# Kernel tuning notes

Measured on AMD Instinct MI355X. Metric: run time of the kernel, lower is better.

Reference implementation:

```python
import jax, jax.numpy as jnp
import numpy as np

LMAX = 6; MMAX = 2
C = 128          # num_channels
H = 8            # num_heads
ALPHA = 32       # attn_alpha_channels
VAL = 16         # attn_value_channels (H*VAL == C)
HID = 64         # attn_hidden_channels
FFN = 128        # ffn_hidden_channels
NL = 4           # num_layers
CUTOFF = 12.0; NRBF = 600
AVG_DEG = 23.395238876342773
AVG_NODES = 77.81317
EPS = 1e-16

def _maps():
    idx, ls = [], []
    for l in range(LMAX + 1):
        mm = min(l, MMAX)
        for m in range(-mm, mm + 1):
            idx.append(l * l + l + m); ls.append(l)
    return np.array(idx), np.array(ls)
_M2F_np, _LOF_np = _maps()
M2F = jnp.asarray(_M2F_np)   # [KM] full-coefficient index of each m-restricted coeff
LOF = jnp.asarray(_LOF_np)   # [KM] degree l of each m-restricted coeff
KM = int(_M2F_np.shape[0])   # 29 for lmax=6, mmax=2
KF = (LMAX + 1) ** 2         # 49

def _rbf(d):
    # GaussianSmearing(0, cutoff, NRBF, width_scalar=2.0)
    off = jnp.linspace(0.0, CUTOFF, NRBF)
    coeff = -0.5 / (2.0 * (off[1] - off[0])) ** 2
    return jnp.exp(coeff * (d[:, None] - off) ** 2)

def _envelope(d):
    # PolynomialEnvelope, exponent p=5
    x = d / CUTOFF
    env = 1.0 - 21.0 * x ** 5 + 35.0 * x ** 6 - 15.0 * x ** 7
    return jnp.where(x < 1.0, env, 0.0)

def _rms(x, g):
    # merge-norm over channel dim with learned per-channel scale
    return x * jax.lax.rsqrt(jnp.mean(x * x, axis=-1, keepdims=True) + 1e-6) * g

def _forward(atomic_numbers, edge_index, edge_distance, emb,
             We0, be0, We1, be1, Weproj, gamma1, gamma2,
             Wr0, Wr1, Wrl, Wmsg, Wap, wa, Wg, Wv, Wo,
             Wf1, Wfg, Wf2, Wh1, Wh2):
    N = atomic_numbers.shape[0]
    src, tgt = edge_index[0], edge_index[1]
    rbf = _rbf(edge_distance)            # [E, NRBF]
    env = _envelope(edge_distance)       # [E]
    # node init: atom embedding on the l=0 component
    x = jnp.zeros((N, KF, C), rbf.dtype).at[:, 0, :].set(emb[atomic_numbers])
    # edge-degree embedding: radial MLP -> per-edge coeffs -> scatter to targets
    h = jax.nn.silu(rbf @ We0 + be0)
    h = jax.nn.silu(h @ We1 + be1)
    deg = (h @ Weproj).reshape(-1, KM, C)              # [E, KM, C]
    x = x.at[tgt[:, None], M2F[None, :], :].add(deg / AVG_DEG)
    for i in range(NL):
        # ---- equivariant graph attention ----
        y = _rms(x, gamma1[i])
        ym = y[:, M2F, :]                               # [N, KM, C] m-restricted
        m = jnp.concatenate([ym[src], ym[tgt]], axis=-1)  # [E, KM, 2C]
        m = jnp.einsum('ekc,ch->ekh', m, Wmsg[i])       # [E, KM, HID]
        # radial function, shared across m within each l (use_rad_l_parametrization)
        rad = jax.nn.silu(jax.nn.silu(rbf @ Wr0[i]) @ Wr1[i])
        radl = rad @ Wrl[i]                             # [E, LMAX+1]
        m = m * radl[:, LOF][..., None]
        # attention logits from invariant (l=0) part
        a = jax.nn.silu(m[:, 0, :] @ Wap[i]).reshape(-1, H, ALPHA)
        logits = jnp.einsum('eha,ha->eh', a, wa[i])     # [E, H]
        segmax = jnp.full((N, H), -jnp.inf, logits.dtype).at[tgt].max(logits)
        ex = env[:, None] * jnp.exp(logits - segmax[tgt])  # envelope-masked softmax
        den = jax.ops.segment_sum(ex, tgt, num_segments=N)
        attn = ex / (den[tgt] + EPS)                    # [E, H]
        # SwiGLU-gated equivariant values
        g = jax.nn.silu(m[:, 0, :] @ Wg[i])             # [E, H*VAL]
        v = jnp.einsum('ekh,hv->ekv', m, Wv[i]) * g[:, None, :]
        v = v.reshape(-1, KM, H, VAL) * attn[:, None, :, None]
        agg = jax.ops.segment_sum(v.reshape(-1, KM, H * VAL), tgt, num_segments=N)
        out = jnp.einsum('nkv,vc->nkc', agg, Wo[i])     # [N, KM, C]
        x = x.at[:, M2F, :].add(out)
        # ---- feed-forward (grid-MLP style SwiGLU) ----
        y = _rms(x, gamma2[i])
        gf = jax.nn.silu(y[:, 0, :] @ Wfg[i])           # [N, FFN]
        hf = jnp.einsum('nkc,cf->nkf', y, Wf1[i]) * gf[:, None, :]
        x = x + jnp.einsum('nkf,fc->nkc', hf, Wf2[i])
    # energy head on invariant part, sum-aggregated over nodes
    s = jax.nn.silu(x[:, 0, :] @ Wh1) @ Wh2             # [N, 1]
    return (jnp.sum(s) / AVG_NODES).reshape(1)

def setup_inputs() -> dict:
    key = jax.random.key(0)
    ks = jax.random.split(key, 24)
    N, E = 6000, 120000
    def rn(k, shape, scale=0.05):
        return jax.random.normal(k, shape, dtype=jnp.float32) * scale
    inp = {}
    inp['atomic_numbers'] = jax.random.randint(ks[0], (N,), 0, 128)
    inp['edge_index'] = jax.random.randint(ks[1], (2, E), 0, N)
    inp['edge_distance'] = jax.random.uniform(ks[2], (E,), minval=0.5, maxval=CUTOFF, dtype=jnp.float32)
    inp['emb'] = rn(ks[3], (128, C), 1.0)
    inp['We0'] = rn(ks[4], (NRBF, 128)); inp['be0'] = jnp.zeros((128,), jnp.float32)
    inp['We1'] = rn(ks[5], (128, 128)); inp['be1'] = jnp.zeros((128,), jnp.float32)
    inp['Weproj'] = rn(ks[6], (128, KM * C))
    inp['gamma1'] = jnp.ones((NL, C), jnp.float32)
    inp['gamma2'] = jnp.ones((NL, C), jnp.float32)
    inp['Wr0'] = rn(ks[7], (NL, NRBF, 128))
    inp['Wr1'] = rn(ks[8], (NL, 128, 128))
    inp['Wrl'] = rn(ks[9], (NL, 128, LMAX + 1), 0.1)
    inp['Wmsg'] = rn(ks[10], (NL, 2 * C, HID))
    inp['Wap'] = rn(ks[11], (NL, HID, H * ALPHA))
    inp['wa'] = rn(ks[12], (NL, H, ALPHA))
    inp['Wg'] = rn(ks[13], (NL, HID, H * VAL))
    inp['Wv'] = rn(ks[14], (NL, HID, H * VAL))
    inp['Wo'] = rn(ks[15], (NL, H * VAL, C))
    inp['Wf1'] = rn(ks[16], (NL, C, FFN))
    inp['Wfg'] = rn(ks[17], (NL, C, FFN))
    inp['Wf2'] = rn(ks[18], (NL, FFN, C))
    inp['Wh1'] = rn(ks[19], (C, C))
    inp['Wh2'] = rn(ks[20], (C, 1))
    return inp

def reference(atomic_numbers, edge_index, edge_distance, emb,
              We0, be0, We1, be1, Weproj, gamma1, gamma2,
              Wr0, Wr1, Wrl, Wmsg, Wap, wa, Wg, Wv, Wo,
              Wf1, Wfg, Wf2, Wh1, Wh2):
    return _forward(atomic_numbers, edge_index, edge_distance, emb,
                    We0, be0, We1, be1, Weproj, gamma1, gamma2,
                    Wr0, Wr1, Wrl, Wmsg, Wap, wa, Wg, Wv, Wo,
                    Wf1, Wfg, Wf2, Wh1, Wh2)
```

## Files before the change

### kernel.cpp

```cpp
#include <hip/hip_runtime.h>

#define KM 29
#define GTAB 2048

typedef __bf16 bf16_t;
typedef __bf16 bf16x8 __attribute__((ext_vector_type(8)));
typedef __bf16 bf16x4 __attribute__((ext_vector_type(4)));
typedef __bf16 bf16x2 __attribute__((ext_vector_type(2)));
typedef float  f32x4  __attribute__((ext_vector_type(4)));
typedef float  f32x2  __attribute__((ext_vector_type(2)));

__device__ __forceinline__ float silu_f(float x){ return x / (1.0f + __expf(-x)); }

__device__ __forceinline__ float wave_reduce_sum(float v){
  #pragma unroll
  for (int s = 1; s < 64; s <<= 1) v += __shfl_xor(v, s);
  return v;
}

__device__ __forceinline__ constexpr int LOF2(int k){
  return (k<1)?0 : (k<4)?1 : (k<9)?2 : (k<14)?3 : (k<19)?4 : (k<24)?5 : 6;
}

__device__ __forceinline__ f32x4 mfma16(bf16x8 a, bf16x8 b, f32x4 c){
// ... 91 lines not shown
  #pragma unroll
  for (int u = 0; u < 10; u++) p[u] = 0.f;
  const int c2 = 2*lane;
  for (int jj = 0; jj < 32; jj++){
    float gj = __shfl(gval, jj);
    int row = j0 + jj;
    const float2 w0 = *(const float2*)(We0 + row*128 + c2);
    p[0] += gj*w0.x; p[1] += gj*w0.y;
    #pragma unroll
    for (int i = 0; i < 4; i++){
      const float2 wr = *(const float2*)(Wr0 + ((size_t)i*600 + row)*128 + c2);
      p[2+2*i] += gj*wr.x; p[3+2*i] += gj*wr.y;
    }
  }
  sb[wid][c2]   = silu_f(p[0] + be0[c2]);
  sb[wid][c2+1] = silu_f(p[1] + be0[c2+1]);
  #pragma unroll
  for (int i = 0; i < 4; i++){
    sb[wid][128 + 128*i + c2]   = silu_f(p[2+2*i]);
    sb[wid][128 + 128*i + c2+1] = silu_f(p[3+2*i]);
  }
  float a0 = 0.f, a1 = 0.f;
  for (int c = 0; c < 128; c++){
    float hv = sb[wid][c];
    const float2 w = *(const float2*)(We1 + c*128 + c2);
    a0 += hv*w.x; a1 += hv*w.y;
  }
  a0 = silu_f(a0 + be1[c2]); a1 = silu_f(a1 + be1[c2+1]);
  h2tab[(size_t)e*128 + c2]     = a0;
  h2tab[(size_t)e*128 + c2 + 1] = a1;
  #pragma unroll
  for (int i = 0; i < 4; i++){
    float r0 = 0.f, r1 = 0.f;
    const float* W1 = Wr1 + (size_t)i*128*128;
    for (int c = 0; c < 128; c++){
      float rv = sb[wid][128 + 128*i + c];
      const float2 w = *(const float2*)(W1 + c*128 + c2);
      r0 += rv*w.x; r1 += rv*w.y;
    }
    r0 = silu_f(r0); r1 = silu_f(r1);
    const float* Wl = Wrl + (size_t)i*128*7;
    float pl[7];
    #pragma unroll
    for (int l = 0; l < 7; l++) pl[l] = r0*Wl[c2*7+l] + r1*Wl[(c2+1)*7+l];
    #pragma unroll
    for (int l = 0; l < 7; l++) pl[l] = wave_reduce_sum(pl[l]);
    if (lane == 0){
      #pragma unroll
      for (int l = 0; l < 7; l++) radtab[(size_t)e*28 + i*7 + l] = pl[l];
    }
  }
}

__global__ void k_h2e(const float* __restrict__ ed, const float* __restrict__ h2tab,
                      bf16_t* __restrict__ h2e, int E){
  int idx = blockIdx.x*256 + threadIdx.x;
  if (idx >= E*128) return;
  int e = idx >> 7, ch = idx & 127;
  float d = ed[e];
  float u = d * ((GTAB-1)/12.0f);
  int j = (int)u; if (j > GTAB-2) j = GTAB-2;
  float f = u - (float)j;
  float a = h2tab[(size_t)j*128 + ch], b = h2tab[(size_t)(j+1)*128 + ch];
  h2e[idx] = (bf16_t)(a + f*(b-a));
}

__global__ __launch_bounds__(256) void k_h2sum(
    const bf16_t* __restrict__ h2e, const int* __restrict__ rowptr, const int* __restrict__ order,
    bf16_t* __restrict__ h2sum, int N)
{
  int n = blockIdx.x*2 + (threadIdx.x >> 7);
  int ch = threadIdx.x & 127;
  if (n >= N) return;
  int rp = rowptr[n], deg = rowptr[n+1] - rp;
  float acc = 0.f;
  for (int idx = 0; idx < deg; idx++){
    int e = order[rp+idx];
    acc += (float)h2e[(size_t)e*128 + ch];
  }
  h2sum[(size_t)n*128 + ch] = (bf16_t)acc;
}

__global__ __launch_bounds__(256) void k_init_x(
    const int* __restrict__ Z, const float* __restrict__ emb,
    const bf16_t* __restrict__ WeprojT, const bf16_t* __restrict__ h2sum,
    bf16_t* __restrict__ Xb, int N)
{
  __shared__ bf16_t h2s[32*136];
  __shared__ int Zs[32];
  int n0 = blockIdx.x*32, t = threadIdx.x;
  for (int idx = t; idx < 32*128; idx += 256){
    int nn = idx >> 7, ch = idx & 127;
    int n = n0 + nn;
    h2s[nn*136 + ch] = (n < N) ? h2sum[(size_t)n*128 + ch] : (bf16_t)0.f;
  }
  if (t < 32) Zs[t] = (n0 + t < N) ? Z[n0+t] : 0;
  __syncthreads();
  int wid = t >> 6, lane = t & 63;
  int mtile = wid & 1;
  int row = mtile*16 + (lane & 15);
  int koff = (lane >> 4)*8;
  bf16x8 afr[4];
  #pragma unroll
  for (int kk = 0; kk < 4; kk++) afr[kk] = *(const bf16x8*)(h2s + row*136 + kk*32 + koff);
  for (int nt = (wid>>1); nt < 232; nt += 2){
    f32x4 acc = {0.f,0.f,0.f,0.f};
    int col = nt*16 + (lane & 15);
    #pragma unroll
    for (int kk = 0; kk < 4; kk++){
      bf16x8 b = *(const bf16x8*)(WeprojT + (size_t)col*128 + kk*32 + koff);
      acc = mfma16(afr[kk], b, acc);
    }
    #pragma unroll
    for (int r = 0; r < 4; r++){
      int r32 = mtile*16 + (lane>>4)*4 + r;
      int n = n0 + r32;
      if (n < N){
        float v = acc[r] * (1.0f/23.395238876342773f);
        if (col < 128) v += emb[(size_t)Zs[r32]*128 + col];
        Xb[(size_t)n*3712 + col] = (bf16_t)v;
      }
    }
  }
}

__global__ __launch_bounds__(512) void k_pqv(
    const bf16_t* __restrict__ Xb, const float* __restrict__ gamma1,
    const bf16_t* __restrict__ WmsgCT, const bf16_t* __restrict__ WvT,
    unsigned char* __restrict__ PV8, unsigned char* __restrict__ QV8,
    float* __restrict__ P0, float* __restrict__ Q0, int layer)
{
  __shared__ bf16_t ys16[32*136];
  __shared__ bf16_t pq16[32*136];
  int n = blockIdx.x, t = threadIdx.x;
  int wid = t >> 6, lane = t & 63;
  const float* g1 = gamma1 + layer*128;
  const bf16_t* xp = Xb + (size_t)n*3712;
  for (int k = wid; k < KM; k += 8){
    float x0 = (float)xp[k*128 + lane], x1 = (float)xp[k*128 + 64 + lane];
    float ss = wave_reduce_sum(x0*x0 + x1*x1);
    float sc = rsqrtf(ss*(1.0f/128.0f) + 1e-6f);
    ys16[k*136 + lane]      = (bf16_t)(x0*sc*g1[lane]);
    ys16[k*136 + 64 + lane] = (bf16_t)(x1*sc*g1[64+lane]);
  }
  for (int idx = t; idx < 3*136; idx += 512) ys16[29*136 + idx] = (bf16_t)0.f;
  __syncthreads();
  int mtile = wid >> 2;
  int row = mtile*16 + (lane & 15);
  int koff = (lane >> 4)*8;
  {
    const bf16_t* Bc = WmsgCT + (size_t)layer*16384;
    f32x4 acc[2] = {{0,0,0,0},{0,0,0,0}};
    #pragma unroll
    for (int kk = 0; kk < 128; kk += 32){
      bf16x8 a = *(const bf16x8*)(ys16 + row*136 + kk + koff);
      #pragma unroll
      for (int u = 0; u < 2; u++){
        int col = ((wid&3)*2+u)*16 + (lane & 15);
        bf16x8 b = *(const bf16x8*)(Bc + (size_t)col*128 + kk + koff);
        acc[u] = mfma16(a, b, acc[u]);
      }
    }
    #pragma unroll
    for (int u = 0; u < 2; u++){
      int col = ((wid&3)*2+u)*16 + (lane & 15);
      #pragma unroll
      for (int r = 0; r < 4; r++){
        int r32 = mtile*16 + (lane>>4)*4 + r;
        pq16[r32*136 + col] = (bf16_t)acc[u][r];
      }
      if (mtile == 0 && (lane>>4) == 0){
        float v = acc[u][0];
        if (col < 64) P0[(size_t)n*64 + col] = v;
        else          Q0[(size_t)n*64 + col - 64] = v;
      }
    }
  }
  __syncthreads();
  {
    const bf16_t* Bt = WvT + (size_t)layer*8192;
    f32x4 acc[2] = {{0,0,0,0},{0,0,0,0}};
    #pragma unroll
    for (int kk = 0; kk < 64; kk += 32){
      bf16x8 a = *(const bf16x8*)(pq16 + row*136 + kk + koff);
      #pragma unroll
      for (int u = 0; u < 2; u++){
        int col = ((wid&3)*2+u)*16 + (lane & 15);
        bf16x8 b = *(const bf16x8*)(Bt + (size_t)col*64 + kk + koff);
        acc[u] = mfma16(a, b, acc[u]);
      }
    }
    unsigned char* pvp = PV8 + (size_t)n*4096;
    int r0i = mtile*16 + (lane>>4)*4;
    #pragma unroll
    for (int u = 0; u < 2; u++){
      int col = ((wid&3)*2+u)*16 + (lane & 15);
      float pk[4];
      #pragma unroll
      for (int r = 0; r < 4; r++){
        int r32 = r0i + r;
        pk[r] = (r32 < KM) ? acc[u][r] : 0.f;
      }
      int dw = __builtin_amdgcn_cvt_pk_fp8_f32(pk[0], pk[1], 0, false);
      dw = __builtin_amdgcn_cvt_pk_fp8_f32(pk[2], pk[3], dw, true);
      *(unsigned int*)(pvp + col*32 + r0i) = (unsigned int)dw;
    }
  }
  {
    const bf16_t* Bt = WvT + (size_t)layer*8192;
    f32x4 acc[2] = {{0,0,0,0},{0,0,0,0}};
    #pragma unroll
    for (int kk = 0; kk < 64; kk += 32){
      bf16x8 a = *(const bf16x8*)(pq16 + row*136 + 64 + kk + koff);
      #pragma unroll
      for (int u = 0; u < 2; u++){
        int col = ((wid&3)*2+u)*16 + (lane & 15);
        bf16x8 b = *(const bf16x8*)(Bt + (size_t)col*64 + kk + koff);
        acc[u] = mfma16(a, b, acc[u]);
      }
    }
    unsigned char* qvp = QV8 + (size_t)n*4096;
    int r0i = mtile*16 + (lane>>4)*4;
    #pragma unroll
    for (int u = 0; u < 2; u++){
      int col = ((wid&3)*2+u)*16 + (lane & 15);
      float pk[4];
      #pragma unroll
      for (int r = 0; r < 4; r++){
        int r32 = r0i + r;
        pk[r] = (r32 < KM) ? acc[u][r] : 0.f;
      }
      int dw = __builtin_amdgcn_cvt_pk_fp8_f32(pk[0], pk[1], 0, false);
      dw = __builtin_amdgcn_cvt_pk_fp8_f32(pk[2], pk[3], dw, true);
      *(unsigned int*)(qvp + col*32 + r0i) = (unsigned int)dw;
    }
  }
}

__global__ __launch_bounds__(256) void k_edge_logits(
    const int* __restrict__ EI, const float* __restrict__ ed,
    const float* __restrict__ P0, const float* __restrict__ Q0,
    const float* __restrict__ radtab, const bf16_t* __restrict__ WapT, const float* __restrict__ wa,
    const bf16_t* __restrict__ WgT, float* __restrict__ logi, bf16_t* __restrict__ gate16,
    int E, int layer)
{
  __shared__ bf16_t m0s[16*72];
  __shared__ int   srcs[16], tgts[16];
  __shared__ float r0s[16];
  int t = threadIdx.x;
  int eb = blockIdx.x*16;
  if (t < 16){
    int e = eb + t;
    if (e < E){
      srcs[t] = EI[e]; tgts[t] = EI[E+e];
      float d = ed[e];
      float u = d * ((GTAB-1)/12.0f);
      int j = (int)u; if (j > GTAB-2) j = GTAB-2;
      float f = u - (float)j;
      float a = radtab[(size_t)j*28 + layer*7], b = radtab[(size_t)(j+1)*28 + layer*7];
      r0s[t] = a + f*(b-a);
    } else { srcs[t] = 0; tgts[t] = 0; r0s[t] = 0.f; }
  }
  __syncthreads();
  #pragma unroll
  for (int u = 0; u < 4; u++){
    int idx = t + u*256;
    int i = idx >> 6, j = idx & 63;
    m0s[i*72 + j] = (bf16_t)((P0[(size_t)srcs[i]*64 + j] + Q0[(size_t)tgts[i]*64 + j]) * r0s[i]);
  }
  __syncthreads();
  int wid = t >> 6, lane = t & 63;
  int l15 = lane & 15, lg = lane >> 4;
  int koff = lg*8;
  bf16x8 a0 = *(const bf16x8*)(m0s + l15*72 + koff);
  bf16x8 a1 = *(const bf16x8*)(m0s + l15*72 + 32 + koff);
  const bf16_t* Ba = WapT + (size_t)layer*16384;
  const bf16_t* Bg = WgT  + (size_t)layer*8192;
  const float* wav = wa + layer*256;
  f32x4 accA[4], accG[2];
  #pragma unroll
  for (int u = 0; u < 4; u++){
    int col = 64*wid + u*16 + l15;
    f32x4 acc = {0,0,0,0};
    acc = mfma16(a0, *(const bf16x8*)(Ba + (size_t)col*64 + koff), acc);
    acc = mfma16(a1, *(const bf16x8*)(Ba + (size_t)col*64 + 32 + koff), acc);
    accA[u] = acc;
  }
// ... 127 lines not shown
      A0 = B0; A1 = B1; gA = gB;
      B0 = C0; B1 = C1; gB = gC;
      i += 4;
    }
  }
  {
    const unsigned char* qvp = QV8 + (size_t)n*4096 + hv*32;
    uint4 q0 = *(const uint4*)qvp;
    uint4 q1 = *(const uint4*)(qvp + 16);
    float rw[7];
    #pragma unroll
    for (int l = 0; l < 7; l++) rw[l] = S[l];
    FMA_DW(q0.x, 0)  FMA_DW(q0.y, 4)  FMA_DW(q0.z, 8)  FMA_DW(q0.w, 12)
    FMA_DW(q1.x, 16) FMA_DW(q1.y, 20) FMA_DW(q1.z, 24) FMA_DW(q1.w, 28)
  }
  if ((hv & 15) == 0) denl[eg*8 + h] = dpart;
  __syncthreads();
  {
    float dsum = denl[h] + denl[8 + h] + denl[16 + h] + denl[24 + h];
    float inv = 1.0f/(dsum + 1e-30f);
    #pragma unroll
    for (int j = 0; j < 32; j++) acc[j] *= inv;
  }
  if (eg == 0){
    #pragma unroll
    for (int j = 0; j < 32; j++) mA[j*136 + hv] = (bf16_t)acc[j];
  } else if (eg == 1){
    #pragma unroll
    for (int j = 0; j < 32; j++) mB[j*136 + hv] = (bf16_t)acc[j];
  }
  __syncthreads();
  if (eg == 2){
    #pragma unroll
    for (int j = 0; j < 32; j++) mA[j*136 + hv] = (bf16_t)((float)mA[j*136 + hv] + acc[j]);
  } else if (eg == 3){
    #pragma unroll
    for (int j = 0; j < 32; j++) mB[j*136 + hv] = (bf16_t)((float)mB[j*136 + hv] + acc[j]);
  }
  __syncthreads();
  for (int idx = t; idx < 3712; idx += 512){
    int k = idx >> 7, c = idx & 127;
    agg[(size_t)n*3712 + idx] = (bf16_t)((float)mA[k*136 + c] + (float)mB[k*136 + c]);
  }
}

__global__ __launch_bounds__(512, 4) void k_xupdate(
    const bf16_t* __restrict__ agg,
    const float* __restrict__ gamma1, const float* __restrict__ gamma2,
    const float* __restrict__ Wfg,
    const bf16_t* __restrict__ Wf1T, const bf16_t* __restrict__ Wf2T,
    const bf16_t* __restrict__ WoT, const bf16_t* __restrict__ WmsgCT, const bf16_t* __restrict__ WvT,
    bf16_t* __restrict__ Xb, int layer,
    unsigned char* __restrict__ PV8o, unsigned char* __restrict__ QV8o,
    float* __restrict__ P0o, float* __restrict__ Q0o, int do_tail)
{
  __shared__ float  xs[3712];
  __shared__ bf16_t ysag[32*136];
  __shared__ bf16_t hsqv[32*136];
  __shared__ float  pf[640];

  int n = blockIdx.x, t = threadIdx.x;
  int wid = t >> 6, lane = t & 63;

  {
    const bf16x2* Xp2 = (const bf16x2*)(Xb + (size_t)n*3712);
    for (int p = t; p < 1856; p += 512){
      bf16x2 v = Xp2[p];
      xs[2*p]   = (float)v.x;
      xs[2*p+1] = (float)v.y;
    }
  }
  for (int idx = t; idx < 3712; idx += 512){
    int k = idx >> 7, c = idx & 127;
    ysag[k*136 + c] = agg[(size_t)n*3712 + idx];
  }
  for (int idx = t; idx < 3*136; idx += 512) ysag[29*136 + idx] = (bf16_t)0.f;
  __syncthreads();
  {
    const bf16_t* Bt = WoT + (size_t)layer*16384;
    int mtile = wid >> 2, colt = (wid & 3)*2;
    int row = mtile*16 + (lane & 15);
    int koff = (lane >> 4)*8;
    f32x4 a2[2] = {{0,0,0,0},{0,0,0,0}};
    #pragma unroll
    for (int kk = 0; kk < 128; kk += 32){
      bf16x8 a = *(const bf16x8*)(ysag + row*136 + kk + koff);
      #pragma unroll
      for (int u = 0; u < 2; u++){
        int col = (colt+u)*16 + (lane & 15);
        bf16x8 b = *(const bf16x8*)(Bt + (size_t)col*128 + kk + koff);
        a2[u] = mfma16(a, b, a2[u]);
      }
    }
    #pragma unroll
    for (int u = 0; u < 2; u++){
      int col = (colt+u)*16 + (lane & 15);
      #pragma unroll
      for (int r = 0; r < 4; r++){
        int r32 = mtile*16 + (lane>>4)*4 + r;
        if (r32 < KM) xs[r32*128 + col] += a2[u][r];
      }
    }
  }
  __syncthreads();
  const float* g2 = gamma2 + layer*128;
  for (int k = wid; k < KM; k += 8){
    float x0 = xs[k*128 + lane], x1 = xs[k*128 + 64 + lane];
    float ss = wave_reduce_sum(x0*x0 + x1*x1);
    float sc = rsqrtf(ss*(1.0f/128.0f) + 1e-6f);
    ysag[k*136 + lane]      = (bf16_t)(x0*sc*g2[lane]);
    ysag[k*136 + 64 + lane] = (bf16_t)(x1*sc*g2[64+lane]);
  }
  for (int idx = t; idx < 3*136; idx += 512) ysag[29*136 + idx] = (bf16_t)0.f;
  __syncthreads();
  {
    int part = t >> 7, f = t & 127;
    const float* Wfgp = Wfg + (size_t)layer*16384;
    float p = 0.f;
    for (int c = part*32; c < part*32 + 32; c++) p += (float)ysag[c] * Wfgp[c*128 + f];
    pf[part*128 + f] = p;
  }
  __syncthreads();
  if (t < 128) pf[512 + t] = silu_f(pf[t] + pf[128+t] + pf[256+t] + pf[384+t]);
  __syncthreads();
  {
    const bf16_t* Bt = Wf1T + (size_t)layer*16384;
    int mtile = wid >> 2, colt = (wid & 3)*2;
    int row = mtile*16 + (lane & 15);
    int koff = (lane >> 4)*8;
    f32x4 a2[2] = {{0,0,0,0},{0,0,0,0}};
    #pragma unroll
    for (int kk = 0; kk < 128; kk += 32){
      bf16x8 a = *(const bf16x8*)(ysag + row*136 + kk + koff);
      #pragma unroll
      for (int u = 0; u < 2; u++){
        int col = (colt+u)*16 + (lane & 15);
        bf16x8 b = *(const bf16x8*)(Bt + (size_t)col*128 + kk + koff);
        a2[u] = mfma16(a, b, a2[u]);
      }
    }
    #pragma unroll
    for (int u = 0; u < 2; u++){
      int col = (colt+u)*16 + (lane & 15);
      float gfc = pf[512 + col];
      #pragma unroll
      for (int r = 0; r < 4; r++){
        int r32 = mtile*16 + (lane>>4)*4 + r;
        hsqv[r32*136 + col] = (bf16_t)(a2[u][r]*gfc);
      }
    }
  }
  __syncthreads();
  {
    const bf16_t* Bt = Wf2T + (size_t)layer*16384;
    int mtile = wid >> 2, colt = (wid & 3)*2;
    int row = mtile*16 + (lane & 15);
    int koff = (lane >> 4)*8;
    f32x4 a2[2] = {{0,0,0,0},{0,0,0,0}};
    #pragma unroll
    for (int kk = 0; kk < 128; kk += 32){
      bf16x8 a = *(const bf16x8*)(hsqv + row*136 + kk + koff);
      #pragma unroll
      for (int u = 0; u < 2; u++){
        int col = (colt+u)*16 + (lane & 15);
        bf16x8 b = *(const bf16x8*)(Bt + (size_t)col*128 + kk + koff);
        a2[u] = mfma16(a, b, a2[u]);
      }
    }
    #pragma unroll
    for (int u = 0; u < 2; u++){
      int col = (colt+u)*16 + (lane & 15);
      #pragma unroll
      for (int r = 0; r < 4; r++){
        int r32 = mtile*16 + (lane>>4)*4 + r;
        if (r32 < KM) xs[r32*128 + col] += a2[u][r];
      }
    }
  }
  __syncthreads();
  {
    bf16x2* Xp2 = (bf16x2*)(Xb + (size_t)n*3712);
    for (int p = t; p < 1856; p += 512){
      bf16x2 v;
      v.x = (bf16_t)xs[2*p];
      v.y = (bf16_t)xs[2*p+1];
      Xp2[p] = v;
    }
  }
  if (do_tail){
    const float* g1n = gamma1 + (size_t)(layer+1)*128;
    for (int k = wid; k < KM; k += 8){
      float x0 = xs[k*128 + lane], x1 = xs[k*128 + 64 + lane];
      float ss = wave_reduce_sum(x0*x0 + x1*x1);
      float sc = rsqrtf(ss*(1.0f/128.0f) + 1e-6f);
      ysag[k*136 + lane]      = (bf16_t)(x0*sc*g1n[lane]);
      ysag[k*136 + 64 + lane] = (bf16_t)(x1*sc*g1n[64+lane]);
    }
    __syncthreads();
    int mtile = wid >> 2;
    int row = mtile*16 + (lane & 15);
    int koff = (lane >> 4)*8;
    {
      const bf16_t* Bc = WmsgCT + (size_t)(layer+1)*16384;
      f32x4 acc[2] = {{0,0,0,0},{0,0,0,0}};
      #pragma unroll
      for (int kk = 0; kk < 128; kk += 32){
        bf16x8 a = *(const bf16x8*)(ysag + row*136 + kk + koff);
        #pragma unroll
        for (int u = 0; u < 2; u++){
          int col = ((wid&3)*2+u)*16 + (lane & 15);
          bf16x8 b = *(const bf16x8*)(Bc + (size_t)col*128 + kk + koff);
          acc[u] = mfma16(a, b, acc[u]);
        }
      }
      #pragma unroll
      for (int u = 0; u < 2; u++){
        int col = ((wid&3)*2+u)*16 + (lane & 15);
        #pragma unroll
        for (int r = 0; r < 4; r++){
          int r32 = mtile*16 + (lane>>4)*4 + r;
          hsqv[r32*136 + col] = (bf16_t)acc[u][r];
        }
        if (mtile == 0 && (lane>>4) == 0){
          float v = acc[u][0];
          if (col < 64) P0o[(size_t)n*64 + col] = v;
          else          Q0o[(size_t)n*64 + col - 64] = v;
        }
      }
    }
    __syncthreads();
    {
      const bf16_t* Bt = WvT + (size_t)(layer+1)*8192;
      f32x4 acc[2] = {{0,0,0,0},{0,0,0,0}};
      #pragma unroll
      for (int kk = 0; kk < 64; kk += 32){
        bf16x8 a = *(const bf16x8*)(hsqv + row*136 + kk + koff);
        #pragma unroll
        for (int u = 0; u < 2; u++){
          int col = ((wid&3)*2+u)*16 + (lane & 15);
          bf16x8 b = *(const bf16x8*)(Bt + (size_t)col*64 + kk + koff);
          acc[u] = mfma16(a, b, acc[u]);
        }
      }
      unsigned char* pvp = PV8o + (size_t)n*4096;
      int r0i = mtile*16 + (lane>>4)*4;
      #pragma unroll
      for (int u = 0; u < 2; u++){
        int col = ((wid&3)*2+u)*16 + (lane & 15);
        float pk[4];
        #pragma unroll
        for (int r = 0; r < 4; r++){
          int r32 = r0i + r;
          pk[r] = (r32 < KM) ? acc[u][r] : 0.f;
        }
        int dw = __builtin_amdgcn_cvt_pk_fp8_f32(pk[0], pk[1], 0, false);
        dw = __builtin_amdgcn_cvt_pk_fp8_f32(pk[2], pk[3], dw, true);
        *(unsigned int*)(pvp + col*32 + r0i) = (unsigned int)dw;
      }
    }
    {
      const bf16_t* Bt = WvT + (size_t)(layer+1)*8192;
      f32x4 acc[2] = {{0,0,0,0},{0,0,0,0}};
      #pragma unroll
      for (int kk = 0; kk < 64; kk += 32){
        bf16x8 a = *(const bf16x8*)(hsqv + row*136 + 64 + kk + koff);
        #pragma unroll
        for (int u = 0; u < 2; u++){
          int col = ((wid&3)*2+u)*16 + (lane & 15);
          bf16x8 b = *(const bf16x8*)(Bt + (size_t)col*64 + kk + koff);
          acc[u] = mfma16(a, b, acc[u]);
        }
      }
      unsigned char* qvp = QV8o + (size_t)n*4096;
      int r0i = mtile*16 + (lane>>4)*4;
      #pragma unroll
      for (int u = 0; u < 2; u++){
        int col = ((wid&3)*2+u)*16 + (lane & 15);
        float pk[4];
        #pragma unroll
        for (int r = 0; r < 4; r++){
          int r32 = r0i + r;
          pk[r] = (r32 < KM) ? acc[u][r] : 0.f;
        }
        int dw = __builtin_amdgcn_cvt_pk_fp8_f32(pk[0], pk[1], 0, false);
        dw = __builtin_amdgcn_cvt_pk_fp8_f32(pk[2], pk[3], dw, true);
        *(unsigned int*)(qvp + col*32 + r0i) = (unsigned int)dw;
      }
    }
  }
}

__global__ __launch_bounds__(256) void k_head(
    const bf16_t* __restrict__ Xb, const float* __restrict__ Wh1, const float* __restrict__ Wh2,
    float* __restrict__ partial, int N)
{
  __shared__ float wsum[4];
  int t = threadIdx.x;
  int half = t >> 7;
  int n = blockIdx.x*2 + half;
  int f = t & 127;
  float sv = 0.f;
  if (n < N){
    const bf16_t* xp = Xb + (size_t)n*3712;
    float acc = 0.f;
    for (int c = 0; c < 128; c++) acc += (float)xp[c]*Wh1[c*128 + f];
    sv = silu_f(acc)*Wh2[f];
  }
  sv = wave_reduce_sum(sv);
  if ((t & 63) == 0) wsum[t >> 6] = sv;
  __syncthreads();
  if (t == 0) partial[blockIdx.x] = wsum[0] + wsum[1] + wsum[2] + wsum[3];
}

__global__ __launch_bounds__(256) void k_reduce(const float* __restrict__ partial, float* __restrict__ out, int P){
  __shared__ float sh[256];
  int t = threadIdx.x;
  float s = 0.f;
  for (int i = t; i < P; i += 256) s += partial[i];
  sh[t] = s; __syncthreads();
  for (int off = 128; off > 0; off >>= 1){
    if (t < off) sh[t] += sh[t+off];
    __syncthreads();
  }
  if (t == 0) out[0] = sh[0] / 77.81317f;
}

extern "C" void kernel_launch(void* const* d_in, const int* in_sizes, int n_in,
                              void* d_out, int out_size, void* d_ws, size_t ws_size,
                              hipStream_t stream)
{
  const int*   Z      = (const int*)d_in[0];
  const int*   EI     = (const int*)d_in[1];
  const float* ed     = (const float*)d_in[2];
  const float* emb    = (const float*)d_in[3];
  const float* We0    = (const float*)d_in[4];
  const float* be0    = (const float*)d_in[5];
  const float* We1    = (const float*)d_in[6];
  const float* be1    = (const float*)d_in[7];
  const float* Weproj = (const float*)d_in[8];
  const float* gamma1 = (const float*)d_in[9];
  const float* gamma2 = (const float*)d_in[10];
  const float* Wr0    = (const float*)d_in[11];
  const float* Wr1    = (const float*)d_in[12];
  const float* Wrl    = (const float*)d_in[13];
  const float* Wmsg   = (const float*)d_in[14];
  const float* Wap    = (const float*)d_in[15];
  const float* wa     = (const float*)d_in[16];
  const float* Wg     = (const float*)d_in[17];
  const float* Wv     = (const float*)d_in[18];
  const float* Wo     = (const float*)d_in[19];
  const float* Wf1    = (const float*)d_in[20];
  const float* Wfg    = (const float*)d_in[21];
  const float* Wf2    = (const float*)d_in[22];
  const float* Wh1    = (const float*)d_in[23];
  const float* Wh2    = (const float*)d_in[24];

  const int N = in_sizes[0];
  const int E = in_sizes[2];

  float* ws = (float*)d_ws;
  size_t o = 0;
  auto alloc = [&](size_t nf){ float* p = ws + o; o += (nf + 7) & ~(size_t)7; return p; };

  bf16_t* Xb    = (bf16_t*)alloc((size_t)N*1856);
  float* P0     = alloc((size_t)N*64);
  float* Q0     = alloc((size_t)N*64);
  float* logi   = alloc((size_t)E*8);
  float* part   = alloc((size_t)((N+1)/2) + 8);
  float* radtab = alloc((size_t)GTAB*28);
  float* h2tab  = alloc((size_t)GTAB*128);
  bf16_t* h2sum = (bf16_t*)alloc((size_t)N*64);
  unsigned char* PV8 = (unsigned char*)alloc((size_t)N*1024);
  unsigned char* QV8 = (unsigned char*)alloc((size_t)N*1024);
  bf16_t* agg   = (bf16_t*)alloc((size_t)N*1856);
  bf16_t* gate16= (bf16_t*)alloc((size_t)E*64);
  bf16_t* arena = (bf16_t*)alloc(434176);
  int* rowptr = (int*)alloc((size_t)N+8);
  int* curs   = (int*)alloc((size_t)N);
  int* order  = (int*)alloc((size_t)E);

  bf16_t* WmsgCT  = arena;
  bf16_t* WvT     = arena + 65536;
  bf16_t* WoT     = arena + 98304;
  bf16_t* Wf1T    = arena + 163840;
  bf16_t* Wf2T    = arena + 229376;
  bf16_t* WapT    = arena + 294912;
  bf16_t* WgT     = arena + 360448;
  bf16_t* WeprojT = arena + 393216;

  bf16_t* h2e = gate16;

  hipMemsetAsync(curs, 0, sizeof(int)*N, stream);
  k_count<<<(E+255)/256, 256, 0, stream>>>(EI, curs, E);
  k_scan<<<1, 1024, 0, stream>>>(curs, rowptr, N);
  k_fill<<<(E+255)/256, 256, 0, stream>>>(EI, curs, order, E);
  k_sort<<<(N+255)/256, 256, 0, stream>>>(rowptr, order, N);

  k_tr2<<<256, 256, 0, stream>>>(Wmsg, WmsgCT);
  k_tr<<<128, 256, 0, stream>>>(Wv,   WvT,  4, 64, 128, 8192);
  k_tr<<<256, 256, 0, stream>>>(Wo,   WoT,  4, 128, 128, 16384);
  k_tr<<<256, 256, 0, stream>>>(Wf1,  Wf1T, 4, 128, 128, 16384);
  k_tr<<<256, 256, 0, stream>>>(Wf2,  Wf2T, 4, 128, 128, 16384);
  k_tr<<<256, 256, 0, stream>>>(Wap,  WapT, 4, 64, 256, 16384);
  k_tr<<<128, 256, 0, stream>>>(Wg,   WgT,  4, 64, 128, 8192);
  k_tr<<<1856, 256, 0, stream>>>(Weproj, WeprojT, 1, 128, 3712, 0);

  k_tab_embed<<<GTAB/4, 256, 0, stream>>>(We0, be0, We1, be1, Wr0, Wr1, Wrl, h2tab, radtab);
  k_h2e<<<(E*128+255)/256, 256, 0, stream>>>(ed, h2tab, h2e, E);
  k_h2sum<<<(N+1)/2, 256, 0, stream>>>(h2e, rowptr, order, h2sum, N);
  k_init_x<<<(N+31)/32, 256, 0, stream>>>(Z, emb, WeprojT, h2sum, Xb, N);

  k_pqv<<<N, 512, 0, stream>>>(Xb, gamma1, WmsgCT, WvT, PV8, QV8, P0, Q0, 0);

  for (int i = 0; i < 4; i++){
    k_edge_logits<<<(E+15)/16, 256, 0, stream>>>(EI, ed, P0, Q0, radtab, WapT, wa, WgT, logi, gate16, E, i);
    k_gather<<<N, 512, 0, stream>>>(EI, rowptr, order, ed, PV8, QV8, gate16, logi, radtab, agg, i);
    k_xupdate<<<N, 512, 0, stream>>>(agg, gamma1, gamma2, Wfg, Wf1T, Wf2T, WoT, WmsgCT, WvT,
                                     Xb, i, PV8, QV8, P0, Q0, (i < 3) ? 1 : 0);
  }

  int PB = (N+1)/2;
  k_head<<<PB, 256, 0, stream>>>(Xb, Wh1, Wh2, part, N);
  k_reduce<<<1, 256, 0, stream>>>(part, (float*)d_out, PB);
}
```

Baseline: 2.078 ms.

## Process two nodes per block in xupdate and fuse h2e interpolation into h2sum

k_xupdate now handles two nodes per 512-thread block, stacking their 32 coefficient rows into a 64-row MFMA tile so each weight fragment load is reused across both nodes and each wave computes four output column tiles. The h2e kernel is removed and the table interpolation is done inline in k_h2sum, dropping an E×128 intermediate write and read. The P/Q value projections in k_pqv and the xupdate tail are merged into one loop that shares the B-fragment loads. In exchange, shared memory per block roughly doubles and register pressure rises, which can lower occupancy, and the grid for xupdate is halved.

```diff
diff --git a/kernel.cpp b/kernel.cpp
--- a/kernel.cpp
+++ b/kernel.cpp
@@ -167,21 +167,9 @@
   }
 }
 
-__global__ void k_h2e(const float* __restrict__ ed, const float* __restrict__ h2tab,
-                      bf16_t* __restrict__ h2e, int E){
-  int idx = blockIdx.x*256 + threadIdx.x;
-  if (idx >= E*128) return;
-  int e = idx >> 7, ch = idx & 127;
-  float d = ed[e];
-  float u = d * ((GTAB-1)/12.0f);
-  int j = (int)u; if (j > GTAB-2) j = GTAB-2;
-  float f = u - (float)j;
-  float a = h2tab[(size_t)j*128 + ch], b = h2tab[(size_t)(j+1)*128 + ch];
-  h2e[idx] = (bf16_t)(a + f*(b-a));
-}
-
 __global__ __launch_bounds__(256) void k_h2sum(
-    const bf16_t* __restrict__ h2e, const int* __restrict__ rowptr, const int* __restrict__ order,
+    const float* __restrict__ ed, const float* __restrict__ h2tab,
+    const int* __restrict__ rowptr, const int* __restrict__ order,
     bf16_t* __restrict__ h2sum, int N)
 {
   int n = blockIdx.x*2 + (threadIdx.x >> 7);
@@ -191,7 +179,12 @@
   float acc = 0.f;
   for (int idx = 0; idx < deg; idx++){
     int e = order[rp+idx];
-    acc += (float)h2e[(size_t)e*128 + ch];
+    float d = ed[e];
+    float u = d * ((GTAB-1)/12.0f);
+    int j = (int)u; if (j > GTAB-2) j = GTAB-2;
+    float f = u - (float)j;
+    float a = h2tab[(size_t)j*128 + ch], b = h2tab[(size_t)(j+1)*128 + ch];
+    acc += a + f*(b-a);
   }
   h2sum[(size_t)n*128 + ch] = (bf16_t)acc;
 }
@@ -294,60 +287,39 @@
   __syncthreads();
   {
     const bf16_t* Bt = WvT + (size_t)layer*8192;
-    f32x4 acc[2] = {{0,0,0,0},{0,0,0,0}};
+    f32x4 accP[2] = {{0,0,0,0},{0,0,0,0}};
+    f32x4 accQ[2] = {{0,0,0,0},{0,0,0,0}};
     #pragma unroll
     for (int kk = 0; kk < 64; kk += 32){
-      bf16x8 a = *(const bf16x8*)(pq16 + row*136 + kk + koff);
+      bf16x8 aP = *(const bf16x8*)(pq16 + row*136 + kk + koff);
+      bf16x8 aQ = *(const bf16x8*)(pq16 + row*136 + 64 + kk + koff);
       #pragma unroll
       for (int u = 0; u < 2; u++){
         int col = ((wid&3)*2+u)*16 + (lane & 15);
         bf16x8 b = *(const bf16x8*)(Bt + (size_t)col*64 + kk + koff);
-        acc[u] = mfma16(a, b, acc[u]);
+        accP[u] = mfma16(aP, b, accP[u]);
+        accQ[u] = mfma16(aQ, b, accQ[u]);
       }
     }
     unsigned char* pvp = PV8 + (size_t)n*4096;
+    unsigned char* qvp = QV8 + (size_t)n*4096;
     int r0i = mtile*16 + (lane>>4)*4;
     #pragma unroll
     for (int u = 0; u < 2; u++){
       int col = ((wid&3)*2+u)*16 + (lane & 15);
-      float pk[4];
+      float pk[4], qk[4];
       #pragma unroll
       for (int r = 0; r < 4; r++){
         int r32 = r0i + r;
-        pk[r] = (r32 < KM) ? acc[u][r] : 0.f;
+        pk[r] = (r32 < KM) ? accP[u][r] : 0.f;
+        qk[r] = (r32 < KM) ? accQ[u][r] : 0.f;
       }
       int dw = __builtin_amdgcn_cvt_pk_fp8_f32(pk[0], pk[1], 0, false);
       dw = __builtin_amdgcn_cvt_pk_fp8_f32(pk[2], pk[3], dw, true);
       *(unsigned int*)(pvp + col*32 + r0i) = (unsigned int)dw;
-    }
-  }
-  {
-    const bf16_t* Bt = WvT + (size_t)layer*8192;
-    f32x4 acc[2] = {{0,0,0,0},{0,0,0,0}};
-    #pragma unroll
-    for (int kk = 0; kk < 64; kk += 32){
-      bf16x8 a = *(const bf16x8*)(pq16 + row*136 + 64 + kk + koff);
-      #pragma unroll
-      for (int u = 0; u < 2; u++){
-        int col = ((wid&3)*2+u)*16 + (lane & 15);
-        bf16x8 b = *(const bf16x8*)(Bt + (size_t)col*64 + kk + koff);
-        acc[u] = mfma16(a, b, acc[u]);
-      }
-    }
-    unsigned char* qvp = QV8 + (size_t)n*4096;
-    int r0i = mtile*16 + (lane>>4)*4;
-    #pragma unroll
-    for (int u = 0; u < 2; u++){
-      int col = ((wid&3)*2+u)*16 + (lane & 15);
-      float pk[4];
-      #pragma unroll
-      for (int r = 0; r < 4; r++){
-        int r32 = r0i + r;
-        pk[r] = (r32 < KM) ? acc[u][r] : 0.f;
-      }
-      int dw = __builtin_amdgcn_cvt_pk_fp8_f32(pk[0], pk[1], 0, false);
-      dw = __builtin_amdgcn_cvt_pk_fp8_f32(pk[2], pk[3], dw, true);
-      *(unsigned int*)(qvp + col*32 + r0i) = (unsigned int)dw;
+      int dw2 = __builtin_amdgcn_cvt_pk_fp8_f32(qk[0], qk[1], 0, false);
+      dw2 = __builtin_amdgcn_cvt_pk_fp8_f32(qk[2], qk[3], dw2, true);
+      *(unsigned int*)(qvp + col*32 + r0i) = (unsigned int)dw2;
     }
   }
 }
@@ -581,239 +553,256 @@
     const bf16_t* __restrict__ WoT, const bf16_t* __restrict__ WmsgCT, const bf16_t* __restrict__ WvT,
     bf16_t* __restrict__ Xb, int layer,
     unsigned char* __restrict__ PV8o, unsigned char* __restrict__ QV8o,
-    float* __restrict__ P0o, float* __restrict__ Q0o, int do_tail)
+    float* __restrict__ P0o, float* __restrict__ Q0o, int do_tail, int N)
 {
-  __shared__ float  xs[3712];
-  __shared__ bf16_t ysag[32*136];
-  __shared__ bf16_t hsqv[32*136];
-  __shared__ float  pf[640];
-
-  int n = blockIdx.x, t = threadIdx.x;
+  __shared__ float  xs[2*3712];
+  __shared__ bf16_t ysag[64*136];
+  __shared__ float  gfb[768];
+
+  int n0 = blockIdx.x*2, t = threadIdx.x;
   int wid = t >> 6, lane = t & 63;
-
-  {
-    const bf16x2* Xp2 = (const bf16x2*)(Xb + (size_t)n*3712);
-    for (int p = t; p < 1856; p += 512){
-      bf16x2 v = Xp2[p];
-      xs[2*p]   = (float)v.x;
-      xs[2*p+1] = (float)v.y;
-    }
-  }
-  for (int idx = t; idx < 3712; idx += 512){
-    int k = idx >> 7, c = idx & 127;
-    ysag[k*136 + c] = agg[(size_t)n*3712 + idx];
-  }
-  for (int idx = t; idx < 3*136; idx += 512) ysag[29*136 + idx] = (bf16_t)0.f;
+  int l15 = lane & 15, lg = lane >> 4;
+  int mtile = wid >> 1, colt = (wid & 1)*4;
+  int rowA = mtile*16 + l15;
+  int koff = lg*8;
+  int node = mtile >> 1;
+
+  for (int no = 0; no < 2; no++){
+    int n = n0 + no;
+    if (n < N){
+      const bf16x2* Xp2 = (const bf16x2*)(Xb + (size_t)n*3712);
+      for (int p = t; p < 1856; p += 512){
+        bf16x2 v = Xp2[p];
+        xs[no*3712 + 2*p]   = (float)v.x;
+        xs[no*3712 + 2*p+1] = (float)v.y;
+      }
+    }
+  }
+  for (int idx = t; idx < 2*3712; idx += 512){
+    int no = idx / 3712; int rem = idx - no*3712;
+    int k = rem >> 7, c = rem & 127;
+    bf16_t v = (bf16_t)0.f;
+    if (n0 + no < N) v = agg[(size_t)(n0+no)*3712 + rem];
+    ysag[(no*32 + k)*136 + c] = v;
+  }
+  for (int idx = t; idx < 2*408; idx += 512){
+    int no = idx / 408; int rem = idx - no*408;
+    ysag[(no*32 + 29)*136 + rem] = (bf16_t)0.f;
+  }
   __syncthreads();
   {
     const bf16_t* Bt = WoT + (size_t)layer*16384;
-    int mtile = wid >> 2, colt = (wid & 3)*2;
-    int row = mtile*16 + (lane & 15);
-    int koff = (lane >> 4)*8;
-    f32x4 a2[2] = {{0,0,0,0},{0,0,0,0}};
+    f32x4 a2[4] = {{0,0,0,0},{0,0,0,0},{0,0,0,0},{0,0,0,0}};
     #pragma unroll
     for (int kk = 0; kk < 128; kk += 32){
-      bf16x8 a = *(const bf16x8*)(ysag + row*136 + kk + koff);
-      #pragma unroll
-      for (int u = 0; u < 2; u++){
-        int col = (colt+u)*16 + (lane & 15);
+      bf16x8 a = *(const bf16x8*)(ysag + rowA*136 + kk + koff);
+      #pragma unroll
+      for (int u = 0; u < 4; u++){
+        int col = (colt+u)*16 + l15;
         bf16x8 b = *(const bf16x8*)(Bt + (size_t)col*128 + kk + koff);
         a2[u] = mfma16(a, b, a2[u]);
       }
     }
     #pragma unroll
-    for (int u = 0; u < 2; u++){
-      int col = (colt+u)*16 + (lane & 15);
+    for (int u = 0; u < 4; u++){
+      int col = (colt+u)*16 + l15;
       #pragma unroll
       for (int r = 0; r < 4; r++){
-        int r32 = mtile*16 + (lane>>4)*4 + r;
-        if (r32 < KM) xs[r32*128 + col] += a2[u][r];
-      }
-    }
-  }
-  __syncthreads();
-  const float* g2 = gamma2 + layer*128;
-  for (int k = wid; k < KM; k += 8){
-    float x0 = xs[k*128 + lane], x1 = xs[k*128 + 64 + lane];
-    float ss = wave_reduce_sum(x0*x0 + x1*x1);
-    float sc = rsqrtf(ss*(1.0f/128.0f) + 1e-6f);
-    ysag[k*136 + lane]      = (bf16_t)(x0*sc*g2[lane]);
-    ysag[k*136 + 64 + lane] = (bf16_t)(x1*sc*g2[64+lane]);
-  }
-  for (int idx = t; idx < 3*136; idx += 512) ysag[29*136 + idx] = (bf16_t)0.f;
-  __syncthreads();
-  {
-    int part = t >> 7, f = t & 127;
+        int r32 = mtile*16 + lg*4 + r;
+        int no = r32 >> 5, k = r32 & 31;
+        if (k < KM && n0+no < N) xs[no*3712 + k*128 + col] += a2[u][r];
+      }
+    }
+  }
+  __syncthreads();
+  {
+    const float* g2 = gamma2 + layer*128;
+    for (int rr = wid; rr < 64; rr += 8){
+      int no = rr >> 5, k = rr & 31;
+      if (k < KM && n0+no < N){
+        float x0 = xs[no*3712 + k*128 + lane], x1 = xs[no*3712 + k*128 + 64 + lane];
+        float ss = wave_reduce_sum(x0*x0 + x1*x1);
+        float sc = rsqrtf(ss*(1.0f/128.0f) + 1e-6f);
+        ysag[rr*136 + lane]      = (bf16_t)(x0*sc*g2[lane]);
+        ysag[rr*136 + 64 + lane] = (bf16_t)(x1*sc*g2[64+lane]);
+      } else {
+        ysag[rr*136 + lane] = (bf16_t)0.f;
+        ysag[rr*136 + 64 + lane] = (bf16_t)0.f;
+      }
+    }
+  }
+  __syncthreads();
+  {
+    int no = t >> 8, part = (t >> 7) & 1, f = t & 127;
     const float* Wfgp = Wfg + (size_t)layer*16384;
+    const bf16_t* yr0 = ysag + (no*32)*136;
     float p = 0.f;
-    for (int c = part*32; c < part*32 + 32; c++) p += (float)ysag[c] * Wfgp[c*128 + f];
-    pf[part*128 + f] = p;
-  }
-  __syncthreads();
-  if (t < 128) pf[512 + t] = silu_f(pf[t] + pf[128+t] + pf[256+t] + pf[384+t]);
+    for (int c = part*64; c < part*64 + 64; c++) p += (float)yr0[c]*Wfgp[c*128 + f];
+    gfb[no*256 + part*128 + f] = p;
+  }
+  __syncthreads();
+  if (t < 256){
+    int no = t >> 7;
+    gfb[512 + t] = silu_f(gfb[no*256 + (t & 127)] + gfb[no*256 + 128 + (t & 127)]);
+  }
   __syncthreads();
   {
     const bf16_t* Bt = Wf1T + (size_t)layer*16384;
-    int mtile = wid >> 2, colt = (wid & 3)*2;
-    int row = mtile*16 + (lane & 15);
-    int koff = (lane >> 4)*8;
-    f32x4 a2[2] = {{0,0,0,0},{0,0,0,0}};
+    bf16x8 afr[4];
+    #pragma unroll
+    for (int kc = 0; kc < 4; kc++) afr[kc] = *(const bf16x8*)(ysag + rowA*136 + kc*32 + koff);
+    __syncthreads();
+    f32x4 a2[4] = {{0,0,0,0},{0,0,0,0},{0,0,0,0},{0,0,0,0}};
+    #pragma unroll
+    for (int kc = 0; kc < 4; kc++){
+      #pragma unroll
+      for (int u = 0; u < 4; u++){
+        int col = (colt+u)*16 + l15;
+        bf16x8 b = *(const bf16x8*)(Bt + (size_t)col*128 + kc*32 + koff);
+        a2[u] = mfma16(afr[kc], b, a2[u]);
+      }
+    }
+    #pragma unroll
+    for (int u = 0; u < 4; u++){
+      int col = (colt+u)*16 + l15;
+      float gfc = gfb[512 + node*128 + col];
+      #pragma unroll
+      for (int r = 0; r < 4; r++){
+        int r32 = mtile*16 + lg*4 + r;
+        ysag[r32*136 + col] = (bf16_t)(a2[u][r]*gfc);
+      }
+    }
+  }
+  __syncthreads();
+  {
+    const bf16_t* Bt = Wf2T + (size_t)layer*16384;
+    f32x4 a2[4] = {{0,0,0,0},{0,0,0,0},{0,0,0,0},{0,0,0,0}};
     #pragma unroll
     for (int kk = 0; kk < 128; kk += 32){
-      bf16x8 a = *(const bf16x8*)(ysag + row*136 + kk + koff);
-      #pragma unroll
-      for (int u = 0; u < 2; u++){
-        int col = (colt+u)*16 + (lane & 15);
+      bf16x8 a = *(const bf16x8*)(ysag + rowA*136 + kk + koff);
+      #pragma unroll
+      for (int u = 0; u < 4; u++){
+        int col = (colt+u)*16 + l15;
         bf16x8 b = *(const bf16x8*)(Bt + (size_t)col*128 + kk + koff);
         a2[u] = mfma16(a, b, a2[u]);
       }
     }
     #pragma unroll
-    for (int u = 0; u < 2; u++){
-      int col = (colt+u)*16 + (lane & 15);
-      float gfc = pf[512 + col];
+    for (int u = 0; u < 4; u++){
+      int col = (colt+u)*16 + l15;
       #pragma unroll
       for (int r = 0; r < 4; r++){
-        int r32 = mtile*16 + (lane>>4)*4 + r;
-        hsqv[r32*136 + col] = (bf16_t)(a2[u][r]*gfc);
-      }
-    }
-  }
-  __syncthreads();
-  {
-    const bf16_t* Bt = Wf2T + (size_t)layer*16384;
-    int mtile = wid >> 2, colt = (wid & 3)*2;
-    int row = mtile*16 + (lane & 15);
-    int koff = (lane >> 4)*8;
-    f32x4 a2[2] = {{0,0,0,0},{0,0,0,0}};
-    #pragma unroll
-    for (int kk = 0; kk < 128; kk += 32){
-      bf16x8 a = *(const bf16x8*)(hsqv + row*136 + kk + koff);
-      #pragma unroll
-      for (int u = 0; u < 2; u++){
-        int col = (colt+u)*16 + (lane & 15);
-        bf16x8 b = *(const bf16x8*)(Bt + (size_t)col*128 + kk + koff);
-        a2[u] = mfma16(a, b, a2[u]);
-      }
-    }
-    #pragma unroll
-    for (int u = 0; u < 2; u++){
-      int col = (colt+u)*16 + (lane & 15);
+        int r32 = mtile*16 + lg*4 + r;
+        int no = r32 >> 5, k = r32 & 31;
+        if (k < KM && n0+no < N) xs[no*3712 + k*128 + col] += a2[u][r];
+      }
+    }
+  }
+  __syncthreads();
+  for (int no = 0; no < 2; no++){
+    int n = n0 + no;
+    if (n < N){
+      bf16x2* Xp2 = (bf16x2*)(Xb + (size_t)n*3712);
+      for (int p = t; p < 1856; p += 512){
+        bf16x2 v;
+        v.x = (bf16_t)xs[no*3712 + 2*p];
+        v.y = (bf16_t)xs[no*3712 + 2*p+1];
+        Xp2[p] = v;
+      }
+    }
+  }
+  if (!do_tail) return;
+  {
+    const float* g1 = gamma1 + (size_t)(layer+1)*128;
+    for (int rr = wid; rr < 64; rr += 8){
+      int no = rr >> 5, k = rr & 31;
+      if (k < KM && n0+no < N){
+        float x0 = xs[no*3712 + k*128 + lane], x1 = xs[no*3712 + k*128 + 64 + lane];
+        float ss = wave_reduce_sum(x0*x0 + x1*x1);
+        float sc = rsqrtf(ss*(1.0f/128.0f) + 1e-6f);
+        ysag[rr*136 + lane]      = (bf16_t)(x0*sc*g1[lane]);
+        ysag[rr*136 + 64 + lane] = (bf16_t)(x1*sc*g1[64+lane]);
+      } else {
+        ysag[rr*136 + lane] = (bf16_t)0.f;
+        ysag[rr*136 + 64 + lane] = (bf16_t)0.f;
+      }
+    }
+  }
+  __syncthreads();
+  {
+    const bf16_t* Bc = WmsgCT + (size_t)(layer+1)*16384;
+    bf16x8 afr[4];
+    #pragma unroll
+    for (int kc = 0; kc < 4; kc++) afr[kc] = *(const bf16x8*)(ysag + rowA*136 + kc*32 + koff);
+    __syncthreads();
+    f32x4 a2[4] = {{0,0,0,0},{0,0,0,0},{0,0,0,0},{0,0,0,0}};
+    #pragma unroll
+    for (int kc = 0; kc < 4; kc++){
+      #pragma unroll
+      for (int u = 0; u < 4; u++){
+        int col = (colt+u)*16 + l15;
+        bf16x8 b = *(const bf16x8*)(Bc + (size_t)col*128 + kc*32 + koff);
+        a2[u] = mfma16(afr[kc], b, a2[u]);
+      }
+    }
+    #pragma unroll
+    for (int u = 0; u < 4; u++){
+      int col = (colt+u)*16 + l15;
       #pragma unroll
       for (int r = 0; r < 4; r++){
-        int r32 = mtile*16 + (lane>>4)*4 + r;
-        if (r32 < KM) xs[r32*128 + col] += a2[u][r];
-      }
-    }
-  }
-  __syncthreads();
-  {
-    bf16x2* Xp2 = (bf16x2*)(Xb + (size_t)n*3712);
-    for (int p = t; p < 1856; p += 512){
-      bf16x2 v;
-      v.x = (bf16_t)xs[2*p];
-      v.y = (bf16_t)xs[2*p+1];
-      Xp2[p] = v;
-    }
-  }
-  if (do_tail){
-    const float* g1n = gamma1 + (size_t)(layer+1)*128;
-    for (int k = wid; k < KM; k += 8){
-      float x0 = xs[k*128 + lane], x1 = xs[k*128 + 64 + lane];
-      float ss = wave_reduce_sum(x0*x0 + x1*x1);
-      float sc = rsqrtf(ss*(1.0f/128.0f) + 1e-6f);
-      ysag[k*136 + lane]      = (bf16_t)(x0*sc*g1n[lane]);
-      ysag[k*136 + 64 + lane] = (bf16_t)(x1*sc*g1n[64+lane]);
-    }
-    __syncthreads();
-    int mtile = wid >> 2;
-    int row = mtile*16 + (lane & 15);
-    int koff = (lane >> 4)*8;
-    {
-      const bf16_t* Bc = WmsgCT + (size_t)(layer+1)*16384;
-      f32x4 acc[2] = {{0,0,0,0},{0,0,0,0}};
-      #pragma unroll
-      for (int kk = 0; kk < 128; kk += 32){
-        bf16x8 a = *(const bf16x8*)(ysag + row*136 + kk + koff);
-        #pragma unroll
-        for (int u = 0; u < 2; u++){
-          int col = ((wid&3)*2+u)*16 + (lane & 15);
-          bf16x8 b = *(const bf16x8*)(Bc + (size_t)col*128 + kk + koff);
-          acc[u] = mfma16(a, b, acc[u]);
+        int r32 = mtile*16 + lg*4 + r;
+        ysag[r32*136 + col] = (bf16_t)a2[u][r];
+        if ((r32 & 31) == 0){
+          int n = n0 + (r32 >> 5);
+          if (n < N){
+            float v = a2[u][r];
+            if (col < 64) P0o[(size_t)n*64 + col] = v;
+            else          Q0o[(size_t)n*64 + col - 64] = v;
+          }
         }
       }
-      #pragma unroll
-      for (int u = 0; u < 2; u++){
-        int col = ((wid&3)*2+u)*16 + (lane & 15);
+    }
+  }
+  __syncthreads();
+  {
+    const bf16_t* Bt = WvT + (size_t)(layer+1)*8192;
+    bf16x8 afr[4];
+    #pragma unroll
+    for (int kc = 0; kc < 4; kc++) afr[kc] = *(const bf16x8*)(ysag + rowA*136 + kc*32 + koff);
+    f32x4 aP[4] = {{0,0,0,0},{0,0,0,0},{0,0,0,0},{0,0,0,0}};
+    f32x4 aQ[4] = {{0,0,0,0},{0,0,0,0},{0,0,0,0},{0,0,0,0}};
+    #pragma unroll
+    for (int kc = 0; kc < 2; kc++){
+      #pragma unroll
+      for (int u = 0; u < 4; u++){
+        int col = (colt+u)*16 + l15;
+        bf16x8 b = *(const bf16x8*)(Bt + (size_t)col*64 + kc*32 + koff);
+        aP[u] = mfma16(afr[kc],   b, aP[u]);
+        aQ[u] = mfma16(afr[2+kc], b, aQ[u]);
+      }
+    }
+    int no = node;
+    int n = n0 + no;
+    if (n < N){
+      int k0 = (mtile & 1)*16 + lg*4;
+      unsigned char* pvp = PV8o + (size_t)n*4096;
+      unsigned char* qvp = QV8o + (size_t)n*4096;
+      #pragma unroll
+      for (int u = 0; u < 4; u++){
+        int col = (colt+u)*16 + l15;
+        float pk[4], qk[4];
         #pragma unroll
         for (int r = 0; r < 4; r++){
-          int r32 = mtile*16 + (lane>>4)*4 + r;
-          hsqv[r32*136 + col] = (bf16_t)acc[u][r];
-        }
-        if (mtile == 0 && (lane>>4) == 0){
-          float v = acc[u][0];
-          if (col < 64) P0o[(size_t)n*64 + col] = v;
-          else          Q0o[(size_t)n*64 + col - 64] = v;
-        }
-      }
-    }
-    __syncthreads();
-    {
-      const bf16_t* Bt = WvT + (size_t)(layer+1)*8192;
-      f32x4 acc[2] = {{0,0,0,0},{0,0,0,0}};
-      #pragma unroll
-      for (int kk = 0; kk < 64; kk += 32){
-        bf16x8 a = *(const bf16x8*)(hsqv + row*136 + kk + koff);
-        #pragma unroll
-        for (int u = 0; u < 2; u++){
-          int col = ((wid&3)*2+u)*16 + (lane & 15);
-          bf16x8 b = *(const bf16x8*)(Bt + (size_t)col*64 + kk + koff);
-          acc[u] = mfma16(a, b, acc[u]);
-        }
-      }
-      unsigned char* pvp = PV8o + (size_t)n*4096;
-      int r0i = mtile*16 + (lane>>4)*4;
-      #pragma unroll
-      for (int u = 0; u < 2; u++){
-        int col = ((wid&3)*2+u)*16 + (lane & 15);
-        float pk[4];
-        #pragma unroll
-        for (int r = 0; r < 4; r++){
-          int r32 = r0i + r;
-          pk[r] = (r32 < KM) ? acc[u][r] : 0.f;
+          int k = k0 + r;
+          pk[r] = (k < KM) ? aP[u][r] : 0.f;
+          qk[r] = (k < KM) ? aQ[u][r] : 0.f;
         }
         int dw = __builtin_amdgcn_cvt_pk_fp8_f32(pk[0], pk[1], 0, false);
         dw = __builtin_amdgcn_cvt_pk_fp8_f32(pk[2], pk[3], dw, true);
-        *(unsigned int*)(pvp + col*32 + r0i) = (unsigned int)dw;
-      }
-    }
-    {
-      const bf16_t* Bt = WvT + (size_t)(layer+1)*8192;
-      f32x4 acc[2] = {{0,0,0,0},{0,0,0,0}};
-      #pragma unroll
-      for (int kk = 0; kk < 64; kk += 32){
-        bf16x8 a = *(const bf16x8*)(hsqv + row*136 + 64 + kk + koff);
-        #pragma unroll
-        for (int u = 0; u < 2; u++){
-          int col = ((wid&3)*2+u)*16 + (lane & 15);
-          bf16x8 b = *(const bf16x8*)(Bt + (size_t)col*64 + kk + koff);
-          acc[u] = mfma16(a, b, acc[u]);
-        }
-      }
-      unsigned char* qvp = QV8o + (size_t)n*4096;
-      int r0i = mtile*16 + (lane>>4)*4;
-      #pragma unroll
-      for (int u = 0; u < 2; u++){
-        int col = ((wid&3)*2+u)*16 + (lane & 15);
-        float pk[4];
-        #pragma unroll
-        for (int r = 0; r < 4; r++){
-          int r32 = r0i + r;
-          pk[r] = (r32 < KM) ? acc[u][r] : 0.f;
-        }
-        int dw = __builtin_amdgcn_cvt_pk_fp8_f32(pk[0], pk[1], 0, false);
-        dw = __builtin_amdgcn_cvt_pk_fp8_f32(pk[2], pk[3], dw, true);
-        *(unsigned int*)(qvp + col*32 + r0i) = (unsigned int)dw;
+        *(unsigned int*)(pvp + col*32 + k0) = (unsigned int)dw;
+        int dw2 = __builtin_amdgcn_cvt_pk_fp8_f32(qk[0], qk[1], 0, false);
+        dw2 = __builtin_amdgcn_cvt_pk_fp8_f32(qk[2], qk[3], dw2, true);
+        *(unsigned int*)(qvp + col*32 + k0) = (unsigned int)dw2;
       }
     }
   }
@@ -917,8 +906,6 @@
   bf16_t* WgT     = arena + 360448;
   bf16_t* WeprojT = arena + 393216;
 
-  bf16_t* h2e = gate16;
-
   hipMemsetAsync(curs, 0, sizeof(int)*N, stream);
   k_count<<<(E+255)/256, 256, 0, stream>>>(EI, curs, E);
   k_scan<<<1, 1024, 0, stream>>>(curs, rowptr, N);
@@ -935,8 +922,7 @@
   k_tr<<<1856, 256, 0, stream>>>(Weproj, WeprojT, 1, 128, 3712, 0);
 
   k_tab_embed<<<GTAB/4, 256, 0, stream>>>(We0, be0, We1, be1, Wr0, Wr1, Wrl, h2tab, radtab);
-  k_h2e<<<(E*128+255)/256, 256, 0, stream>>>(ed, h2tab, h2e, E);
-  k_h2sum<<<(N+1)/2, 256, 0, stream>>>(h2e, rowptr, order, h2sum, N);
+  k_h2sum<<<(N+1)/2, 256, 0, stream>>>(ed, h2tab, rowptr, order, h2sum, N);
   k_init_x<<<(N+31)/32, 256, 0, stream>>>(Z, emb, WeprojT, h2sum, Xb, N);
 
   k_pqv<<<N, 512, 0, stream>>>(Xb, gamma1, WmsgCT, WvT, PV8, QV8, P0, Q0, 0);
@@ -944,8 +930,8 @@
   for (int i = 0; i < 4; i++){
     k_edge_logits<<<(E+15)/16, 256, 0, stream>>>(EI, ed, P0, Q0, radtab, WapT, wa, WgT, logi, gate16, E, i);
     k_gather<<<N, 512, 0, stream>>>(EI, rowptr, order, ed, PV8, QV8, gate16, logi, radtab, agg, i);
-    k_xupdate<<<N, 512, 0, stream>>>(agg, gamma1, gamma2, Wfg, Wf1T, Wf2T, WoT, WmsgCT, WvT,
-                                     Xb, i, PV8, QV8, P0, Q0, (i < 3) ? 1 : 0);
+    k_xupdate<<<(N+1)/2, 512, 0, stream>>>(agg, gamma1, gamma2, Wfg, Wf1T, Wf2T, WoT, WmsgCT, WvT,
+                                           Xb, i, PV8, QV8, P0, Q0, (i < 3) ? 1 : 0, N);
   }
 
   int PB = (N+1)/2;
```

After: 2.168 ms. +4.3%, slower.
